# Kernel tuning notes

Measured on AMD Instinct MI355X. Metric: run time of the kernel, lower is better.

## Reference

```python
import jax, jax.numpy as jnp
import numpy as np

HEADS = 8
DIM_HEAD = 64
DIM = 512
B, N = 4, 2048
SCALE = DIM_HEAD ** -0.5


def setup_inputs() -> dict:
    key = jax.random.key(0)
    k1, k2, k3, k4, k5, k6 = jax.random.split(key, 6)
    inner = HEADS * DIM_HEAD
    s = DIM ** -0.5
    return {
        "input_feature": jax.random.normal(k1, (B, N, DIM), dtype=jnp.float32),
        "mask": jax.random.randint(k2, (B, N), 0, 2, dtype=jnp.int32),
        "Wq": jax.random.normal(k3, (inner, DIM), dtype=jnp.float32) * s,
        "Wk": jax.random.normal(k4, (inner, DIM), dtype=jnp.float32) * s,
        "Wv": jax.random.normal(k5, (inner, DIM), dtype=jnp.float32) * s,
        "Wout": jax.random.normal(k6, (DIM, inner), dtype=jnp.float32) * s,
    }


def reference(input_feature, mask, Wq, Wk, Wv, Wout):
    # Conv1d with kernel_size=1, no bias == per-token linear: out = W @ x_channels
    q = jnp.einsum('bnc,dc->bnd', input_feature, Wq)  # [B, N, H*Dh]
    k = jnp.einsum('bnc,dc->bnd', input_feature, Wk)
    v = jnp.einsum('bnc,dc->bnd', input_feature, Wv)

    # '(n c)' channel layout is head-major -> reshape to [B, N, H, Dh], move head out front
    def split_heads(t):
        return t.reshape(B, N, HEADS, DIM_HEAD).transpose(2, 0, 1, 3)  # [H, B, N, Dh]

    q, k, v = split_heads(q), split_heads(k), split_heads(v)

    scores = jnp.einsum('hbtd,hbsd->hbts', q, k) * SCALE  # [H, B, N, N]
    # masked_fill(mask == 0, 1e-9): fill with small CONSTANT (not -inf), faithful to source
    m = (mask == 0)[None, :, None, :]  # [1, B, 1, N]
    scores = jnp.where(m, jnp.float32(1e-9), scores)
    att = jax.nn.softmax(scores, axis=-1)
    out = jnp.einsum('hbts,hbsd->hbtd', att, v)  # [H, B, N, Dh]

    # '(n b) tokens c -> b (n c) tokens' : head-major channel concat
    out = out.transpose(1, 2, 0, 3).reshape(B, N, HEADS * DIM_HEAD)  # [B, N, H*Dh]
    out = jnp.einsum('bnd,ed->bne', out, Wout)  # [B, N, DIM]
    return out
```

## Files before the change

### kernel.cpp

```cpp
#include <hip/hip_runtime.h>
#include <hip/hip_bf16.h>

typedef __attribute__((ext_vector_type(8))) short short8;
typedef __attribute__((ext_vector_type(4))) short short4_t;
typedef __attribute__((ext_vector_type(4))) float float4_;

#define LOG2E 1.4426950408889634f

__device__ __forceinline__ short f2bf(float f) {
    unsigned int u = __builtin_bit_cast(unsigned int, f);
    u = (u + 0x7FFFu + ((u >> 16) & 1u)) >> 16;
    return (short)u;
}

__device__ __forceinline__ unsigned pk2bf(float a, float b) {
    unsigned ua = __builtin_bit_cast(unsigned, a) + 0x8000u;
    unsigned ub = __builtin_bit_cast(unsigned, b) + 0x8000u;
    return __builtin_amdgcn_perm(ub, ua, 0x07060302);
}

__device__ __forceinline__ void gload_lds16(const short* g, short* l) {
    __builtin_amdgcn_global_load_lds((const __attribute__((address_space(1))) void*)g,
                                     (__attribute__((address_space(3))) void*)l, 16, 0, 0);
}

__global__ __launch_bounds__(256) void cvt_kernel(
    const float* __restrict__ X, const float* __restrict__ Wq, const float* __restrict__ Wk,
    const float* __restrict__ Wv, const float* __restrict__ Wo,
    short* __restrict__ Xb, short* __restrict__ Wqkvb, short* __restrict__ Wob) {
    int i = blockIdx.x * 256 + threadIdx.x;
    const float* src; short* dst; float sc = 1.0f;
    if (i < 1048576) { src = X + (size_t)i * 4; dst = Xb + (size_t)i * 4; }
    else {
        int w = i - 1048576; int sec = w >> 16; int j = (w & 65535) * 4;
        if (sec == 0)      { src = Wq + j; dst = Wqkvb + j; sc = 0.125f * LOG2E; }
        else if (sec == 1) { src = Wk + j; dst = Wqkvb + 262144 + j; }
        else if (sec == 2) { src = Wv + j; dst = Wqkvb + 524288 + j; }
        else               { src = Wo + j; dst = Wob + j; }
    }
    float4 v = *(const float4*)src;
    short4_t o;
    o[0] = f2bf(v.x * sc); o[1] = f2bf(v.y * sc); o[2] = f2bf(v.z * sc); o[3] = f2bf(v.w * sc);
    *(short4_t*)dst = o;
}

__global__ __launch_bounds__(256) void gemm_qkv(const short* __restrict__ A, const short* __restrict__ B,
                                                const int* __restrict__ mask,
                                                short* __restrict__ Qb, short* __restrict__ Kb,
                                                short* __restrict__ Vtb) {
    __shared__ __align__(16) short smemAB[2 * 8192];
    __shared__ int maskL[128];
    short* At = smemAB;
    short* Bt = smemAB + 8192;
    constexpr int K = 512;
    int tid = threadIdx.x;
    int wid = tid >> 6, lane = tid & 63;
    int quad = lane >> 4, cc = lane & 15;
    int c7 = cc & 7;
    int wr = wid >> 1, wc = wid & 1;
    int m0 = blockIdx.y * 128, n0 = blockIdx.x * 128;
    if (tid < 128) maskL[tid] = mask[m0 + tid];

    const short* gA[4]; const short* gB[4]; int lofs[4];
#pragma unroll
    for (int p = 0; p < 4; ++p) {
        int slot = p * 256 + tid;
        int r = slot >> 3, c = slot & 7;
        int cs = (c ^ (r & 7)) * 8;
        gA[p] = A + (size_t)(m0 + r) * K + cs;
        gB[p] = B + (size_t)(n0 + r) * K + cs;
        lofs[p] = slot * 8;
    }
    short8 arg[4], brg[4];
#pragma unroll
    for (int p = 0; p < 4; ++p) { arg[p] = *(const short8*)gA[p]; brg[p] = *(const short8*)gB[p]; }

    float4_ acc[4][4] = {};

    for (int kk = 0; kk < K; kk += 64) {
        __syncthreads();
#pragma unroll
        for (int p = 0; p < 4; ++p) {
            *(short8*)(At + lofs[p]) = arg[p];
            *(short8*)(Bt + lofs[p]) = brg[p];
        }
        if (kk < K - 64) {
#pragma unroll
            for (int p = 0; p < 4; ++p) {
                arg[p] = *(const short8*)(gA[p] + kk + 64);
                brg[p] = *(const short8*)(gB[p] + kk + 64);
            }
        }
        __syncthreads();
#pragma unroll
        for (int kc = 0; kc < 2; ++kc) {
            short8 af[4], bf[4];
#pragma unroll
            for (int i = 0; i < 4; ++i)
                af[i] = *(const short8*)(At + (wr * 64 + i * 16 + cc) * 64 + (((kc * 4 + quad) ^ c7) * 8));
#pragma unroll
            for (int j = 0; j < 4; ++j)
                bf[j] = *(const short8*)(Bt + (wc * 64 + j * 16 + cc) * 64 + (((kc * 4 + quad) ^ c7) * 8));
#pragma unroll
            for (int i = 0; i < 4; ++i)
#pragma unroll
                for (int j = 0; j < 4; ++j)
                    acc[i][j] = __builtin_amdgcn_mfma_f32_16x16x32_bf16(af[i], bf[j], acc[i][j], 0, 0, 0);
        }
    }

    int which = n0 >> 9;
    int b = m0 >> 11;
    if (which == 2) {
        __syncthreads();
        short* T = smemAB;
#pragma unroll
        for (int i = 0; i < 4; ++i) {
#pragma unroll
            for (int j = 0; j < 4; ++j) {
                int d_l = wc * 64 + j * 16 + cc;
                int nnb = wr * 64 + i * 16 + quad * 4;
                int G = nnb >> 3, half = (nnb >> 2) & 1;
                int Gs = G ^ (d_l & 15);
                short4_t pv;
                pv[0] = f2bf(acc[i][j][0]); pv[1] = f2bf(acc[i][j][1]);
                pv[2] = f2bf(acc[i][j][2]); pv[3] = f2bf(acc[i][j][3]);
                *(short4_t*)(T + d_l * 128 + Gs * 8 + half * 4) = pv;
            }
        }
        __syncthreads();
#pragma unroll
        for (int p = 0; p < 8; ++p) {
            int slot = p * 256 + tid;
            int d = slot >> 4, G = slot & 15;
            short8 v = *(const short8*)(T + d * 128 + ((G ^ (d & 15)) * 8));
            *(short8*)(Vtb + ((size_t)(b * 512 + (n0 & 511) + d)) * 2048 + (m0 & 2047) + G * 8) = v;
        }
    } else {
        short* dst = which ? Kb : Qb;
#pragma unroll
        for (int i = 0; i < 4; ++i) {
#pragma unroll
            for (int j = 0; j < 4; ++j) {
#pragma unroll
                for (int r = 0; r < 4; ++r) {
                    int lm = wr * 64 + i * 16 + quad * 4 + r;
                    int nn = (m0 & 2047) + lm;
                    int hd = (n0 & 511) + wc * 64 + j * 16 + cc;
                    int h = hd >> 6, dh = hd & 63;
                    float v = acc[i][j][r];
                    if (which == 1 && maskL[lm] == 0) v = 0.0f;
                    dst[((((size_t)b * 8 + h) * 2048 + nn) * 64) + dh] = f2bf(v);
                }
            }
        }
    }
}

__global__ __launch_bounds__(256, 4) void attn_kernel(const short* __restrict__ Q, const short* __restrict__ Kg,
                                                      const short* __restrict__ Vt,
                                                      short* __restrict__ AO) {
    __shared__ __align__(16) char smem[40960];
    short* KbufL = (short*)smem;
    short* VbufL = (short*)(smem + 16384);
    short* Pt    = (short*)(smem + 32768);
    float* Lw    = (float*)smem;
    float* Lfin  = (float*)(smem + 1024);

    int tid = threadIdx.x;
    int w = tid >> 6, lane = tid & 63;
    int quad = lane >> 4, cc = lane & 15;
    int tg = w >> 1, dh = w & 1;
    int bh = blockIdx.x, b = bh >> 3, h = bh & 7;
    int t0 = blockIdx.y * 64;
    size_t kbase = (size_t)bh * 2048 * 64;
    size_t vbase = (size_t)b * 512 * 2048 + (size_t)h * 64 * 2048;

    short8 qf[4][2];
#pragma unroll
    for (int tb = 0; tb < 4; ++tb)
#pragma unroll
        for (int kc = 0; kc < 2; ++kc)
            qf[tb][kc] = *(const short8*)(Q + kbase + (size_t)(t0 + tb * 16 + cc) * 64 + kc * 32 + quad * 8);

    int c7 = cc & 7;
    int koff[2], poff_w[4], aoff[2][2], voff[2][2];
#pragma unroll
    for (int kc = 0; kc < 2; ++kc)
        koff[kc] = (w * 16 + cc) * 64 + (((kc * 4 + quad) ^ c7) * 8);
#pragma unroll
    for (int tb = 0; tb < 4; ++tb)
        poff_w[tb] = (tb * 16 + cc) * 64 + (((w * 2 + (quad >> 1)) ^ c7) * 8) + (quad & 1) * 4;
#pragma unroll
    for (int mb = 0; mb < 2; ++mb)
#pragma unroll
        for (int kc = 0; kc < 2; ++kc)
            aoff[mb][kc] = (tg * 32 + mb * 16 + cc) * 64 + (((kc * 4 + quad) ^ c7) * 8);
#pragma unroll
    for (int db = 0; db < 2; ++db)
#pragma unroll
        for (int kc = 0; kc < 2; ++kc)
            voff[db][kc] = (dh * 32 + db * 16 + cc) * 64 + (((kc * 4 + quad) ^ c7) * 8);

    float4_ o[2][2] = {};
    float lp[4] = {0.f, 0.f, 0.f, 0.f};

    int sA = tid >> 3, cA = tid & 7;
    const short* gK0 = Kg + kbase + (size_t)sA * 64 + ((cA ^ (sA & 7)) * 8);
    const short* gK1 = gK0 + 32 * 64;
    const short* gV0 = Vt + vbase + (size_t)sA * 2048 + ((cA ^ (sA & 7)) * 8);
    const short* gV1 = gV0 + 32 * 2048;
    int ld0 = tid * 8, ld1 = tid * 8 + 2048;

    short8 krg0 = *(const short8*)gK0, krg1 = *(const short8*)gK1;
    short8 vrg0 = *(const short8*)gV0, vrg1 = *(const short8*)gV1;
    gK0 += 4096; gK1 += 4096; gV0 += 64; gV1 += 64;
    *(short8*)(KbufL + ld0) = krg0; *(short8*)(KbufL + ld1) = krg1;
    *(short8*)(VbufL + ld0) = vrg0; *(short8*)(VbufL + ld1) = vrg1;
    krg0 = *(const short8*)gK0; krg1 = *(const short8*)gK1;
    vrg0 = *(const short8*)gV0; vrg1 = *(const short8*)gV1;
    gK0 += 4096; gK1 += 4096; gV0 += 64; gV1 += 64;

    for (int it = 0; it < 32; ++it) {
        int cur = it & 1;
        const short* Kt  = KbufL + cur * 4096;
        const short* Vtt = VbufL + cur * 4096;
        __syncthreads();

        if (it < 31) {
            short* Kn = KbufL + (cur ^ 1) * 4096;
            short* Vn = VbufL + (cur ^ 1) * 4096;
            *(short8*)(Kn + ld0) = krg0; *(short8*)(Kn + ld1) = krg1;
            *(short8*)(Vn + ld0) = vrg0; *(short8*)(Vn + ld1) = vrg1;
        }
        if (it < 30) {
            krg0 = *(const short8*)gK0; krg1 = *(const short8*)gK1;
            vrg0 = *(const short8*)gV0; vrg1 = *(const short8*)gV1;
            gK0 += 4096; gK1 += 4096; gV0 += 64; gV1 += 64;
        }

        short8 kf0 = *(const short8*)(Kt + koff[0]);
        short8 kf1 = *(const short8*)(Kt + koff[1]);
        float4_ acc[4];
#pragma unroll
        for (int tb = 0; tb < 4; ++tb) {
            float4_ a = {0.f, 0.f, 0.f, 0.f};
            a = __builtin_amdgcn_mfma_f32_16x16x32_bf16(kf0, qf[tb][0], a, 0, 0, 0);
            a = __builtin_amdgcn_mfma_f32_16x16x32_bf16(kf1, qf[tb][1], a, 0, 0, 0);
            acc[tb] = a;
        }
#pragma unroll
        for (int tb = 0; tb < 4; ++tb) {
            float x0 = __builtin_amdgcn_exp2f(acc[tb][0]);
            float x1 = __builtin_amdgcn_exp2f(acc[tb][1]);
            float x2 = __builtin_amdgcn_exp2f(acc[tb][2]);
            float x3 = __builtin_amdgcn_exp2f(acc[tb][3]);
            lp[tb] += (x0 + x1) + (x2 + x3);
            uint2 pw; pw.x = pk2bf(x0, x1); pw.y = pk2bf(x2, x3);
            *(uint2*)(Pt + poff_w[tb]) = pw;
        }
        __syncthreads();

        short8 af[2][2], vf[2][2];
#pragma unroll
        for (int mb = 0; mb < 2; ++mb)
#pragma unroll
            for (int kc = 0; kc < 2; ++kc)
                af[mb][kc] = *(const short8*)(Pt + aoff[mb][kc]);
#pragma unroll
        for (int db = 0; db < 2; ++db)
#pragma unroll
            for (int kc = 0; kc < 2; ++kc)
                vf[db][kc] = *(const short8*)(Vtt + voff[db][kc]);
#pragma unroll
        for (int mb = 0; mb < 2; ++mb)
#pragma unroll
            for (int db = 0; db < 2; ++db) {
                o[mb][db] = __builtin_amdgcn_mfma_f32_16x16x32_bf16(af[mb][0], vf[db][0], o[mb][db], 0, 0, 0);
                o[mb][db] = __builtin_amdgcn_mfma_f32_16x16x32_bf16(af[mb][1], vf[db][1], o[mb][db], 0, 0, 0);
            }
    }

#pragma unroll
    for (int tb = 0; tb < 4; ++tb) {
        lp[tb] += __shfl_xor(lp[tb], 16, 64);
        lp[tb] += __shfl_xor(lp[tb], 32, 64);
    }
    __syncthreads();
    if (lane < 16) {
#pragma unroll
        for (int tb = 0; tb < 4; ++tb) Lw[w * 64 + tb * 16 + lane] = lp[tb];
    }
    __syncthreads();
    if (tid < 64) {
        float s = Lw[tid] + Lw[64 + tid] + Lw[128 + tid] + Lw[192 + tid];
        Lfin[tid] = 1.0f / s;
    }
    __syncthreads();

#pragma unroll
    for (int mb = 0; mb < 2; ++mb)
#pragma unroll
        for (int r = 0; r < 4; ++r) {
            int tl = tg * 32 + mb * 16 + quad * 4 + r;
            float inv = Lfin[tl];
            size_t rowbase = ((size_t)(b * 2048 + t0 + tl)) * 512 + h * 64;
#pragma unroll
            for (int db = 0; db < 2; ++db)
                AO[rowbase + dh * 32 + db * 16 + cc] = f2bf(o[mb][db][r] * inv);
        }
}

__global__ __launch_bounds__(256) void gemm_out(const short* __restrict__ A, const short* __restrict__ B,
                                                float* __restrict__ C) {
    __shared__ short At[64 * 64];
    __shared__ short Bt[64 * 64];
    constexpr int K = 512;
    int tid = threadIdx.x;
    int wid = tid >> 6, lane = tid & 63;
    int quad = lane >> 4, cc = lane & 15;
    int c7 = cc & 7;
    int wr = wid >> 1, wc = wid & 1;
    int m0 = blockIdx.y * 64, n0 = blockIdx.x * 64;

    float4_ acc[2][2] = {};

    for (int kk = 0; kk < K; kk += 64) {
#pragma unroll
        for (int p = 0; p < 2; ++p) {
            int slot = p * 256 + tid;
            int r = slot >> 3, c = slot & 7;
            int cs = (c ^ (r & 7)) * 8;
            gload_lds16(A + (size_t)(m0 + r) * K + kk + cs, At + slot * 8);
            gload_lds16(B + (size_t)(n0 + r) * K + kk + cs, Bt + slot * 8);
        }
        __syncthreads();
#pragma unroll
        for (int kc = 0; kc < 2; ++kc) {
            short8 af[2], bf[2];
#pragma unroll
            for (int i = 0; i < 2; ++i)
                af[i] = *(const short8*)(At + (wr * 32 + i * 16 + cc) * 64 + (((kc * 4 + quad) ^ c7) * 8));
#pragma unroll
            for (int j = 0; j < 2; ++j)
                bf[j] = *(const short8*)(Bt + (wc * 32 + j * 16 + cc) * 64 + (((kc * 4 + quad) ^ c7) * 8));
#pragma unroll
            for (int i = 0; i < 2; ++i)
#pragma unroll
                for (int j = 0; j < 2; ++j)
                    acc[i][j] = __builtin_amdgcn_mfma_f32_16x16x32_bf16(af[i], bf[j], acc[i][j], 0, 0, 0);
        }
        __syncthreads();
    }

#pragma unroll
    for (int i = 0; i < 2; ++i)
#pragma unroll
        for (int j = 0; j < 2; ++j)
#pragma unroll
            for (int r = 0; r < 4; ++r) {
                int gm = m0 + wr * 32 + i * 16 + quad * 4 + r;
                int gn = n0 + wc * 32 + j * 16 + cc;
                C[(size_t)gm * 512 + gn] = acc[i][j][r];
            }
}

extern "C" void kernel_launch(void* const* d_in, const int* in_sizes, int n_in,
                              void* d_out, int out_size, void* d_ws, size_t ws_size,
                              hipStream_t stream) {
    const float* X  = (const float*)d_in[0];
    const int* mask = (const int*)d_in[1];
    const float* Wq = (const float*)d_in[2];
    const float* Wk = (const float*)d_in[3];
    const float* Wv = (const float*)d_in[4];
    const float* Wo = (const float*)d_in[5];

    char* ws = (char*)d_ws;
    short* Xbf   = (short*)(ws + 0);
    short* Wqkvb = (short*)(ws + 8388608);
    short* Wob   = (short*)(ws + 9961472);
    short* Qb    = (short*)(ws + 10485760);
    short* Kb    = (short*)(ws + 18874368);
    short* Vtb   = (short*)(ws + 27262976);
    short* AOb   = (short*)(ws + 35651584);

    cvt_kernel<<<5120, 256, 0, stream>>>(X, Wq, Wk, Wv, Wo, Xbf, Wqkvb, Wob);
    gemm_qkv<<<dim3(12, 64), 256, 0, stream>>>(Xbf, Wqkvb, mask, Qb, Kb, Vtb);
    attn_kernel<<<dim3(32, 32), 256, 0, stream>>>(Qb, Kb, Vtb, AOb);
    gemm_out<<<dim3(8, 128), 256, 0, stream>>>(AOb, Wob, (float*)d_out);
}
```

Baseline: 165.0 us.

## Restructure attention so each wave owns 32 queries and keeps P in registers

The attention kernel now gives each wave its own 32 query rows across all 64 keys of a tile. Probabilities are rearranged into MFMA operand layout with permlane32/16 swaps, so the LDS round trip for P and one barrier per iteration go away. V fragments are loaded straight from global memory into double-buffered registers instead of being staged in LDS. The block covers 128 queries, the grid is halved, launch bounds drop to 2 blocks per CU, and setprio hints are added around the MFMA work. In exchange, register pressure rises and V loads are no longer shared between waves through LDS.

New measurement: 182.8 us. +10.8%, slower.

```diff
diff --git a/kernel.cpp b/kernel.cpp
--- a/kernel.cpp
+++ b/kernel.cpp
@@ -18,6 +18,17 @@
     unsigned ub = __builtin_bit_cast(unsigned, b) + 0x8000u;
     return __builtin_amdgcn_perm(ub, ua, 0x07060302);
 }
+
+__device__ __forceinline__ void pl32swap(unsigned &a, unsigned &b) {
+    auto r = __builtin_amdgcn_permlane32_swap(a, b, false, false);
+    a = r[0]; b = r[1];
+}
+__device__ __forceinline__ void pl16swap(unsigned &a, unsigned &b) {
+    auto r = __builtin_amdgcn_permlane16_swap(a, b, false, false);
+    a = r[0]; b = r[1];
+}
+
+union U4 { unsigned u[4]; short8 s; };
 
 __device__ __forceinline__ void gload_lds16(const short* g, short* l) {
     __builtin_amdgcn_global_load_lds((const __attribute__((address_space(1))) void*)g,
@@ -157,157 +168,154 @@
     }
 }
 
-__global__ __launch_bounds__(256, 4) void attn_kernel(const short* __restrict__ Q, const short* __restrict__ Kg,
+__global__ __launch_bounds__(256, 2) void attn_kernel(const short* __restrict__ Q, const short* __restrict__ Kg,
                                                       const short* __restrict__ Vt,
                                                       short* __restrict__ AO) {
-    __shared__ __align__(16) char smem[40960];
-    short* KbufL = (short*)smem;
-    short* VbufL = (short*)(smem + 16384);
-    short* Pt    = (short*)(smem + 32768);
-    float* Lw    = (float*)smem;
-    float* Lfin  = (float*)(smem + 1024);
+    __shared__ __align__(16) short KbufL[2 * 4096];
 
     int tid = threadIdx.x;
     int w = tid >> 6, lane = tid & 63;
     int quad = lane >> 4, cc = lane & 15;
-    int tg = w >> 1, dh = w & 1;
+    int c7 = cc & 7;
     int bh = blockIdx.x, b = bh >> 3, h = bh & 7;
-    int t0 = blockIdx.y * 64;
+    int t0 = blockIdx.y * 128 + w * 32;
     size_t kbase = (size_t)bh * 2048 * 64;
     size_t vbase = (size_t)b * 512 * 2048 + (size_t)h * 64 * 2048;
 
-    short8 qf[4][2];
-#pragma unroll
-    for (int tb = 0; tb < 4; ++tb)
+    short8 qf[2][2];
+#pragma unroll
+    for (int tb = 0; tb < 2; ++tb)
 #pragma unroll
         for (int kc = 0; kc < 2; ++kc)
             qf[tb][kc] = *(const short8*)(Q + kbase + (size_t)(t0 + tb * 16 + cc) * 64 + kc * 32 + quad * 8);
 
-    int c7 = cc & 7;
-    int koff[2], poff_w[4], aoff[2][2], voff[2][2];
-#pragma unroll
-    for (int kc = 0; kc < 2; ++kc)
-        koff[kc] = (w * 16 + cc) * 64 + (((kc * 4 + quad) ^ c7) * 8);
-#pragma unroll
-    for (int tb = 0; tb < 4; ++tb)
-        poff_w[tb] = (tb * 16 + cc) * 64 + (((w * 2 + (quad >> 1)) ^ c7) * 8) + (quad & 1) * 4;
-#pragma unroll
-    for (int mb = 0; mb < 2; ++mb)
+    int koff[4][2];
+#pragma unroll
+    for (int sb = 0; sb < 4; ++sb)
 #pragma unroll
         for (int kc = 0; kc < 2; ++kc)
-            aoff[mb][kc] = (tg * 32 + mb * 16 + cc) * 64 + (((kc * 4 + quad) ^ c7) * 8);
-#pragma unroll
-    for (int db = 0; db < 2; ++db)
-#pragma unroll
-        for (int kc = 0; kc < 2; ++kc)
-            voff[db][kc] = (dh * 32 + db * 16 + cc) * 64 + (((kc * 4 + quad) ^ c7) * 8);
-
-    float4_ o[2][2] = {};
-    float lp[4] = {0.f, 0.f, 0.f, 0.f};
+            koff[sb][kc] = (sb * 16 + cc) * 64 + (((kc * 4 + quad) ^ c7) * 8);
 
     int sA = tid >> 3, cA = tid & 7;
     const short* gK0 = Kg + kbase + (size_t)sA * 64 + ((cA ^ (sA & 7)) * 8);
     const short* gK1 = gK0 + 32 * 64;
-    const short* gV0 = Vt + vbase + (size_t)sA * 2048 + ((cA ^ (sA & 7)) * 8);
-    const short* gV1 = gV0 + 32 * 2048;
     int ld0 = tid * 8, ld1 = tid * 8 + 2048;
-
     short8 krg0 = *(const short8*)gK0, krg1 = *(const short8*)gK1;
-    short8 vrg0 = *(const short8*)gV0, vrg1 = *(const short8*)gV1;
-    gK0 += 4096; gK1 += 4096; gV0 += 64; gV1 += 64;
+    gK0 += 4096; gK1 += 4096;
     *(short8*)(KbufL + ld0) = krg0; *(short8*)(KbufL + ld1) = krg1;
-    *(short8*)(VbufL + ld0) = vrg0; *(short8*)(VbufL + ld1) = vrg1;
     krg0 = *(const short8*)gK0; krg1 = *(const short8*)gK1;
-    vrg0 = *(const short8*)gV0; vrg1 = *(const short8*)gV1;
-    gK0 += 4096; gK1 += 4096; gV0 += 64; gV1 += 64;
-
-    for (int it = 0; it < 32; ++it) {
+    gK0 += 4096; gK1 += 4096;
+
+    const short* gVb = Vt + vbase + (size_t)cc * 2048 + quad * 8;
+    short8 vfA[4][2], vfB[4][2];
+#pragma unroll
+    for (int db = 0; db < 4; ++db)
+#pragma unroll
+        for (int kc = 0; kc < 2; ++kc)
+            vfA[db][kc] = *(const short8*)(gVb + db * 32768 + kc * 32);
+
+    float4_ o[2][4] = {};
+    float lp[2] = {0.f, 0.f};
+
+    auto body = [&](short8 (&vfc)[4][2], short8 (&vfn)[4][2], int it) {
+        __syncthreads();
         int cur = it & 1;
-        const short* Kt  = KbufL + cur * 4096;
-        const short* Vtt = VbufL + cur * 4096;
-        __syncthreads();
-
+        const short* Kt = KbufL + cur * 4096;
         if (it < 31) {
             short* Kn = KbufL + (cur ^ 1) * 4096;
-            short* Vn = VbufL + (cur ^ 1) * 4096;
-            *(short8*)(Kn + ld0) = krg0; *(short8*)(Kn + ld1) = krg1;
-            *(short8*)(Vn + ld0) = vrg0; *(short8*)(Vn + ld1) = vrg1;
+            *(short8*)(Kn + ld0) = krg0;
+            *(short8*)(Kn + ld1) = krg1;
         }
         if (it < 30) {
             krg0 = *(const short8*)gK0; krg1 = *(const short8*)gK1;
-            vrg0 = *(const short8*)gV0; vrg1 = *(const short8*)gV1;
-            gK0 += 4096; gK1 += 4096; gV0 += 64; gV1 += 64;
-        }
-
-        short8 kf0 = *(const short8*)(Kt + koff[0]);
-        short8 kf1 = *(const short8*)(Kt + koff[1]);
-        float4_ acc[4];
-#pragma unroll
-        for (int tb = 0; tb < 4; ++tb) {
-            float4_ a = {0.f, 0.f, 0.f, 0.f};
-            a = __builtin_amdgcn_mfma_f32_16x16x32_bf16(kf0, qf[tb][0], a, 0, 0, 0);
-            a = __builtin_amdgcn_mfma_f32_16x16x32_bf16(kf1, qf[tb][1], a, 0, 0, 0);
-            acc[tb] = a;
-        }
-#pragma unroll
-        for (int tb = 0; tb < 4; ++tb) {
-            float x0 = __builtin_amdgcn_exp2f(acc[tb][0]);
-            float x1 = __builtin_amdgcn_exp2f(acc[tb][1]);
-            float x2 = __builtin_amdgcn_exp2f(acc[tb][2]);
-            float x3 = __builtin_amdgcn_exp2f(acc[tb][3]);
-            lp[tb] += (x0 + x1) + (x2 + x3);
-            uint2 pw; pw.x = pk2bf(x0, x1); pw.y = pk2bf(x2, x3);
-            *(uint2*)(Pt + poff_w[tb]) = pw;
-        }
-        __syncthreads();
-
-        short8 af[2][2], vf[2][2];
-#pragma unroll
-        for (int mb = 0; mb < 2; ++mb)
-#pragma unroll
-            for (int kc = 0; kc < 2; ++kc)
-                af[mb][kc] = *(const short8*)(Pt + aoff[mb][kc]);
-#pragma unroll
-        for (int db = 0; db < 2; ++db)
-#pragma unroll
-            for (int kc = 0; kc < 2; ++kc)
-                vf[db][kc] = *(const short8*)(Vtt + voff[db][kc]);
-#pragma unroll
-        for (int mb = 0; mb < 2; ++mb)
-#pragma unroll
-            for (int db = 0; db < 2; ++db) {
-                o[mb][db] = __builtin_amdgcn_mfma_f32_16x16x32_bf16(af[mb][0], vf[db][0], o[mb][db], 0, 0, 0);
-                o[mb][db] = __builtin_amdgcn_mfma_f32_16x16x32_bf16(af[mb][1], vf[db][1], o[mb][db], 0, 0, 0);
-            }
-    }
-
-#pragma unroll
-    for (int tb = 0; tb < 4; ++tb) {
-        lp[tb] += __shfl_xor(lp[tb], 16, 64);
-        lp[tb] += __shfl_xor(lp[tb], 32, 64);
-    }
-    __syncthreads();
-    if (lane < 16) {
-#pragma unroll
-        for (int tb = 0; tb < 4; ++tb) Lw[w * 64 + tb * 16 + lane] = lp[tb];
-    }
-    __syncthreads();
-    if (tid < 64) {
-        float s = Lw[tid] + Lw[64 + tid] + Lw[128 + tid] + Lw[192 + tid];
-        Lfin[tid] = 1.0f / s;
-    }
-    __syncthreads();
-
-#pragma unroll
-    for (int mb = 0; mb < 2; ++mb)
+            gK0 += 4096; gK1 += 4096;
+        }
+        if (it < 31) {
+            int s1 = (it + 1) * 64;
+#pragma unroll
+            for (int db = 0; db < 4; ++db)
+#pragma unroll
+                for (int kc = 0; kc < 2; ++kc)
+                    vfn[db][kc] = *(const short8*)(gVb + db * 32768 + kc * 32 + s1);
+        }
+
+        float4_ acc[4][2];
+        __builtin_amdgcn_s_setprio(1);
+#pragma unroll
+        for (int sb = 0; sb < 4; ++sb) {
+            short8 kf0 = *(const short8*)(Kt + koff[sb][0]);
+            short8 kf1 = *(const short8*)(Kt + koff[sb][1]);
+#pragma unroll
+            for (int tb = 0; tb < 2; ++tb) {
+                float4_ z = {0.f, 0.f, 0.f, 0.f};
+                z = __builtin_amdgcn_mfma_f32_16x16x32_bf16(kf0, qf[tb][0], z, 0, 0, 0);
+                acc[sb][tb] = __builtin_amdgcn_mfma_f32_16x16x32_bf16(kf1, qf[tb][1], z, 0, 0, 0);
+            }
+        }
+        __builtin_amdgcn_s_setprio(0);
+
+        unsigned Wp[4][2][2];
+#pragma unroll
+        for (int sb = 0; sb < 4; ++sb)
+#pragma unroll
+            for (int tb = 0; tb < 2; ++tb) {
+                float x0 = __builtin_amdgcn_exp2f(acc[sb][tb][0]);
+                float x1 = __builtin_amdgcn_exp2f(acc[sb][tb][1]);
+                float x2 = __builtin_amdgcn_exp2f(acc[sb][tb][2]);
+                float x3 = __builtin_amdgcn_exp2f(acc[sb][tb][3]);
+                lp[tb] += (x0 + x1) + (x2 + x3);
+                Wp[sb][tb][0] = pk2bf(x0, x1);
+                Wp[sb][tb][1] = pk2bf(x2, x3);
+            }
+
+        short8 pa[2][2];
+#pragma unroll
+        for (int kc = 0; kc < 2; ++kc)
+#pragma unroll
+            for (int tb = 0; tb < 2; ++tb) {
+                unsigned a0 = Wp[2 * kc][tb][0], a1 = Wp[2 * kc][tb][1];
+                unsigned b0 = Wp[2 * kc + 1][tb][0], b1 = Wp[2 * kc + 1][tb][1];
+                pl32swap(a0, b0); pl32swap(a1, b1);
+                pl16swap(a0, b0); pl16swap(a1, b1);
+                U4 u; u.u[0] = a0; u.u[1] = a1; u.u[2] = b0; u.u[3] = b1;
+                pa[tb][kc] = u.s;
+            }
+
+        __builtin_amdgcn_s_setprio(1);
+#pragma unroll
+        for (int db = 0; db < 4; ++db)
+#pragma unroll
+            for (int tb = 0; tb < 2; ++tb) {
+                o[tb][db] = __builtin_amdgcn_mfma_f32_16x16x32_bf16(pa[tb][0], vfc[db][0], o[tb][db], 0, 0, 0);
+                o[tb][db] = __builtin_amdgcn_mfma_f32_16x16x32_bf16(pa[tb][1], vfc[db][1], o[tb][db], 0, 0, 0);
+            }
+        __builtin_amdgcn_s_setprio(0);
+    };
+
+#pragma unroll 1
+    for (int it = 0; it < 32; it += 2) {
+        body(vfA, vfB, it);
+        body(vfB, vfA, it + 1);
+    }
+
+    float inv[2];
+#pragma unroll
+    for (int tb = 0; tb < 2; ++tb) {
+        float s = lp[tb];
+        s += __shfl_xor(s, 16, 64);
+        s += __shfl_xor(s, 32, 64);
+        inv[tb] = 1.0f / s;
+    }
+#pragma unroll
+    for (int tb = 0; tb < 2; ++tb)
 #pragma unroll
         for (int r = 0; r < 4; ++r) {
-            int tl = tg * 32 + mb * 16 + quad * 4 + r;
-            float inv = Lfin[tl];
+            int tl = tb * 16 + quad * 4 + r;
+            float iv = __shfl(inv[tb], quad * 4 + r, 64);
             size_t rowbase = ((size_t)(b * 2048 + t0 + tl)) * 512 + h * 64;
 #pragma unroll
-            for (int db = 0; db < 2; ++db)
-                AO[rowbase + dh * 32 + db * 16 + cc] = f2bf(o[mb][db][r] * inv);
+            for (int db = 0; db < 4; ++db)
+                AO[rowbase + db * 16 + cc] = f2bf(o[tb][db][r] * iv);
         }
 }
 
@@ -386,6 +394,6 @@
 
     cvt_kernel<<<5120, 256, 0, stream>>>(X, Wq, Wk, Wv, Wo, Xbf, Wqkvb, Wob);
     gemm_qkv<<<dim3(12, 64), 256, 0, stream>>>(Xbf, Wqkvb, mask, Qb, Kb, Vtb);
-    attn_kernel<<<dim3(32, 32), 256, 0, stream>>>(Qb, Kb, Vtb, AOb);
+    attn_kernel<<<dim3(32, 16), 256, 0, stream>>>(Qb, Kb, Vtb, AOb);
     gemm_out<<<dim3(8, 128), 256, 0, stream>>>(AOb, Wob, (float*)d_out);
 }
```
